# Kernel optimization log

Hardware: AMD Instinct MI355X
Metric: run time of the kernel (lower is better)

Reference implementation:

```python
import jax, jax.numpy as jnp
import numpy as np

N_HEAD, D_MODEL, D_HEAD = 16, 1024, 64
SEQ, BATCH = 2048, 2
EPS = 1e-5


def layer_norm(x, g, b):
    mu = jnp.mean(x, axis=-1, keepdims=True)
    var = jnp.var(x, axis=-1, keepdims=True)
    return (x - mu) * jax.lax.rsqrt(var + EPS) * g + b


def pos_table(n_rows, d_model):
    pos = jnp.arange(n_rows, dtype=jnp.float32)[:, None]
    freqs = jnp.power(10000.0, -jnp.arange(0, d_model, 2, dtype=jnp.float32) / d_model)
    ang = pos * freqs  # [n_rows, d_model//2]
    tab = jnp.zeros((n_rows, d_model), dtype=jnp.float32)
    tab = tab.at[:, 0::2].set(jnp.sin(ang))
    tab = tab.at[:, 1::2].set(jnp.cos(ang))
    return tab


def setup_inputs() -> dict:
    key = jax.random.key(0)
    ks = jax.random.split(key, 7)
    s = 0.02
    return {
        "dec_inp": jax.random.normal(ks[0], (SEQ, BATCH, D_MODEL), jnp.float32),
        "Wq": jax.random.normal(ks[1], (N_HEAD * D_HEAD, D_MODEL), jnp.float32) * s,
        "Wkv": jax.random.normal(ks[2], (2 * N_HEAD * D_HEAD, D_MODEL), jnp.float32) * s,
        "Wo": jax.random.normal(ks[3], (D_MODEL, N_HEAD * D_HEAD), jnp.float32) * s,
        "g1": jnp.ones((D_MODEL,), jnp.float32),
        "b1": jnp.zeros((D_MODEL,), jnp.float32),
        "Wff": jax.random.normal(ks[4], (D_MODEL, N_HEAD * D_HEAD), jnp.float32) * s,
        "g2": jnp.ones((D_MODEL,), jnp.float32),
        "b2": jnp.zeros((D_MODEL,), jnp.float32),
    }


def reference(dec_inp, Wq, Wkv, Wo, g1, b1, Wff, g2, b2):
    S, B, D = dec_inp.shape
    scale = 1.0 / (D_HEAD ** 0.5)
    # projections (post-lnorm path, no mems: c == h)
    q = jnp.einsum('ibd,ed->ibe', dec_inp, Wq).reshape(S, B, N_HEAD, D_HEAD)
    kv = jnp.einsum('ibd,ed->ibe', dec_inp, Wkv)
    k, v = jnp.split(kv, 2, axis=-1)
    k = k.reshape(S, B, N_HEAD, D_HEAD)
    v = v.reshape(S, B, N_HEAD, D_HEAD)
    # attention: scores [i, j, b, n], softmax over j (dim=1)
    scores = jnp.einsum('ibnd,jbnd->ijbn', q, k) * scale
    prob = jax.nn.softmax(scores, axis=1)
    vec = jnp.einsum('ijbn,jbnd->ibnd', prob, v).reshape(S, B, N_HEAD * D_HEAD)
    attn_out = jnp.einsum('ibe,de->ibd', vec, Wo)
    out = layer_norm(dec_inp + attn_out, g1, b1)
    # output += ff(output)
    out = out + jnp.einsum('ibe,de->ibd', out, Wff)
    out = layer_norm(out, g2, b2)
    # output += pos_emb(output)  ==  2*out + pe  (pe indexed by shape[1]==batch)
    pe = pos_table(B, D)  # [B, D], broadcasts over seq
    return out + (out + pe)
```

## Files before the change

### kernel.cpp

```cpp
#include <hip/hip_runtime.h>
#include <hip/hip_bf16.h>
#include <math.h>


typedef __bf16 bf16x8 __attribute__((ext_vector_type(8)));
typedef float f32x4  __attribute__((ext_vector_type(4)));

typedef const __attribute__((address_space(1))) unsigned int as1_uint;
typedef __attribute__((address_space(3))) unsigned int as3_uint;

constexpr int S_SEQ = 2048;
constexpr int DH    = 64;

#define WS_MB (1ull << 20)

__device__ __forceinline__ void gload16(void* lds, const void* g) {
  __builtin_amdgcn_global_load_lds((as1_uint*)g, (as3_uint*)lds, 16, 0, 0);
}

__device__ __forceinline__ float fast_exp2(float x) {
  float r;
  asm volatile("v_exp_f32 %0, %1\n\ts_nop 1" : "=v"(r) : "v"(x));
  return r;
}
__device__ __forceinline__ unsigned cvt_pk_bf16(float lo, float hi) {
  unsigned r;
  asm("v_cvt_pk_bf16_f32 %0, %1, %2" : "=v"(r) : "v"(lo), "v"(hi));
  return r;
}

__device__ __forceinline__ void cvt4(const float* __restrict__ in,
                                     __hip_bfloat16* __restrict__ out, int idx) {
  float4 v = ((const float4*)in)[idx];
  uint2 p;
  p.x = cvt_pk_bf16(v.x, v.y);
  p.y = cvt_pk_bf16(v.z, v.w);
  *(uint2*)(out + (size_t)idx * 4) = p;
}

__global__ __launch_bounds__(256)
void prep_kernel(const float* __restrict__ x, const float* __restrict__ Wq,
                 const float* __restrict__ Wkv, const float* __restrict__ Wo,
                 const float* __restrict__ Wff,
                 __hip_bfloat16* __restrict__ Xb,
                 __hip_bfloat16* __restrict__ Wqkv_b,
                 __hip_bfloat16* __restrict__ Wo_b,
                 __hip_bfloat16* __restrict__ Wff_b,
                 float* __restrict__ pe) {
  const int bid = blockIdx.x, t = threadIdx.x;
  if (bid < 4096) {
    cvt4(x, Xb, bid * 256 + t);
  } else if (bid < 5120) {
    cvt4(Wq, Wqkv_b, (bid - 4096) * 256 + t);
  } else if (bid < 7168) {
    cvt4(Wkv, Wqkv_b + 1024 * 1024, (bid - 5120) * 256 + t);
  } else if (bid < 8192) {
    cvt4(Wo, Wo_b, (bid - 7168) * 256 + t);
  } else if (bid < 9216) {
    cvt4(Wff, Wff_b, (bid - 8192) * 256 + t);
  } else {
#pragma unroll
    for (int rep = 0; rep < 2; ++rep) {
      const int k = rep * 256 + t;
      float freq = expf(-(2.0f * (float)k / 1024.0f) * logf(10000.0f));
      pe[2 * k]            = 0.0f;
      pe[2 * k + 1]        = 1.0f;
      pe[1024 + 2 * k]     = sinf(freq);
      pe[1024 + 2 * k + 1] = cosf(freq);
    }
  }
}

template <int MODE, int BN>
__global__ __launch_bounds__(256)
void gemm_bt(const __hip_bfloat16* __restrict__ A,
             const __hip_bfloat16* __restrict__ Bw,
             float* __restrict__ C,
             __hip_bfloat16* __restrict__ Qb,
             __hip_bfloat16* __restrict__ Kb,
             __hip_bfloat16* __restrict__ VTb,
             int Ndim, int Kdim) {
  constexpr int ASZ = 128 * 64 * 2;
  constexpr int BSZ = BN * 64 * 2;
  constexpr int NI  = BN / 32;
  __shared__ __align__(16) char smem[2 * (ASZ + BSZ)];
  const int t = threadIdx.x, w = t >> 6, l = t & 63;
  const int bm = blockIdx.y * 128, bn = blockIdx.x * BN;
  const int m0 = (w >> 1) * 64, n0 = (w & 1) * (BN / 2);
  const int lrow = l >> 3, lcol = l & 7;
  const int ll = l & 15, lg = l >> 4;

  auto stage = [&](char* buf, int kt) {
#pragma unroll
    for (int r = 0; r < 4; ++r) {
      const int chunk = r * 4 + w;
      const int row = chunk * 8 + lrow;
      gload16(buf + chunk * 1024 + l * 16,
              A + (size_t)(bm + row) * Kdim + kt + lcol * 8);
    }
#pragma unroll
    for (int r = 0; r < BN / 32; ++r) {
      const int chunk = r * 4 + w;
      const int row = chunk * 8 + lrow;
      gload16(buf + ASZ + chunk * 1024 + l * 16,
              Bw + (size_t)(bn + row) * Kdim + kt + lcol * 8);
    }
  };

  f32x4 acc[4][NI] = {};

  stage(smem, 0);
  __syncthreads();
  int cur = 0;
  for (int kt = 0; kt < Kdim; kt += 64) {
    char* bufc = smem + cur * (ASZ + BSZ);
    if (kt + 64 < Kdim) stage(smem + (cur ^ 1) * (ASZ + BSZ), kt + 64);
    const char* sA = bufc;
    const char* sB = bufc + ASZ;
#pragma unroll
    for (int ks = 0; ks < 2; ++ks) {
      bf16x8 a[4], bfr[NI];
#pragma unroll
      for (int mi = 0; mi < 4; ++mi)
        a[mi] = *(const bf16x8*)(sA + (m0 + mi * 16 + ll) * 128 + ks * 64 + lg * 16);
#pragma unroll
      for (int ni = 0; ni < NI; ++ni)
        bfr[ni] = *(const bf16x8*)(sB + (n0 + ni * 16 + ll) * 128 + ks * 64 + lg * 16);
#pragma unroll
      for (int mi = 0; mi < 4; ++mi)
#pragma unroll
        for (int ni = 0; ni < NI; ++ni)
          acc[mi][ni] = __builtin_amdgcn_mfma_f32_16x16x32_bf16(
              a[mi], bfr[ni], acc[mi][ni], 0, 0, 0);
    }
    __syncthreads();
    cur ^= 1;
  }

  if (MODE == 0) {
#pragma unroll
    for (int mi = 0; mi < 4; ++mi)
#pragma unroll
      for (int ni = 0; ni < NI; ++ni)
#pragma unroll
        for (int r = 0; r < 4; ++r) {
          const int gm = bm + m0 + mi * 16 + lg * 4 + r;
          const int gn = bn + n0 + ni * 16 + ll;
          C[(size_t)gm * Ndim + gn] = acc[mi][ni][r];
        }
  } else {
    __hip_bfloat16* img = (__hip_bfloat16*)smem;
    const bool isV = (bn >= 2048);
#pragma unroll
    for (int mi = 0; mi < 4; ++mi)
#pragma unroll
      for (int ni = 0; ni < NI; ++ni)
#pragma unroll
        for (int r = 0; r < 4; ++r) {
          const int gml = m0 + mi * 16 + lg * 4 + r;
          const int gnl = n0 + ni * 16 + ll;
          const int off = isV ? gnl * 136 + ((gml & 1) << 6) + (gml >> 1)
                              : gml * 136 + gnl;
          img[off] = __float2bfloat16(acc[mi][ni][r]);
        }
    __syncthreads();
    const int i0 = bm >> 1;
    const int tile0 = bm >> 6;
#pragma unroll
    for (int j = 0; j < 8; ++j) {
      const int c = j * 256 + t;
      uint4 val;
      __hip_bfloat16* dst;
      if (bn < 1024) {
        const int bb = c >> 10, hl = (c >> 9) & 1;
        const int q = c & 511, il = q >> 3, dh0 = (q & 7) * 8;
        val = *(const uint4*)&img[(il * 2 + bb) * 136 + hl * 64 + dh0];
        dst = Qb + ((size_t)(bb * 16 + (bn >> 6) + hl) * 2048 + i0 + il) * 64 + dh0;
      } else if (bn < 2048) {
        const int run = c >> 6, lane = c & 63;
        const int bb = run >> 4, hl = (run >> 3) & 1, th = (run >> 2) & 1,
                  instr = run & 3;
        const int lg2 = lane >> 4, ll2 = lane & 15;
        const int r32 = (ll2 >> 2) * 8 + (ll2 & 3) + ((instr >> 1) << 2);
        const int il = th * 32 + r32;
        const int dh0 = (instr & 1) * 32 + lg2 * 8;
        val = *(const uint4*)&img[(il * 2 + bb) * 136 + hl * 64 + dh0];
        dst = Kb + (size_t)(bb * 16 + ((bn - 1024) >> 6) + hl) * 131072 +
              (size_t)(tile0 + th) * 2048 + instr * 512 + lane * 8;
      } else {
        const int run = c >> 6, lane = c & 63;
        const int bb = run >> 4, hl = (run >> 3) & 1, th = (run >> 2) & 1,
                  df = run & 3;
        const int lg2 = lane >> 4, ll2 = lane & 15;
        const int il0 = th * 32 + lg2 * 8;
        const int gnl = hl * 64 + df * 16 + ll2;
        val = *(const uint4*)&img[gnl * 136 + bb * 64 + il0];
        dst = VTb + (size_t)(bb * 16 + ((bn - 2048) >> 6) + hl) * 131072 +
              (size_t)(tile0 + th) * 2048 + df * 512 + lane * 8;
      }
      *(uint4*)dst = val;
    }
  }
}


#define MFMA_B16 __builtin_amdgcn_mfma_f32_16x16x32_bf16

#define STAGE2(bufp, cb)                                                      \
  {                                                                           \
    gload16((bufp) + woff, Kf + (cb) + wl16);                                 \
    gload16((bufp) + 4096 + woff, Vf + (cb) + wl16);                          \
    gload16((bufp) + 8192 + woff, Kf + (cb) + 4096 + wl16);                   \
    gload16((bufp) + 12288 + woff, Vf + (cb) + 4096 + wl16);                  \
  }

#define COMPUTE(cur)                                                          \
  {                                                                           \
    bf16x8 kk[4], vv[4];                                                      \
    _Pragma("unroll")                                                         \
    for (int i = 0; i < 4; ++i) {                                             \
      kk[i] = *(const bf16x8*)((cur) + i * 1024 + l16);                       \
      vv[i] = *(const bf16x8*)((cur) + 4096 + i * 1024 + l16);                \
    }                                                                         \
    const f32x4 z = {0.f, 0.f, 0.f, 0.f};                                     \
    f32x4 s0[2], s1[2];                                                       \
    __builtin_amdgcn_s_setprio(1);                                            \
    s0[0] = MFMA_B16(kk[0], qf[0][0], z, 0, 0, 0);                            \
    s0[0] = MFMA_B16(kk[1], qf[0][1], s0[0], 0, 0, 0);                        \
    s1[0] = MFMA_B16(kk[2], qf[0][0], z, 0, 0, 0);                            \
    s1[0] = MFMA_B16(kk[3], qf[0][1], s1[0], 0, 0, 0);                        \
    s0[1] = MFMA_B16(kk[0], qf[1][0], z, 0, 0, 0);                            \
    s0[1] = MFMA_B16(kk[1], qf[1][1], s0[1], 0, 0, 0);                        \
    s1[1] = MFMA_B16(kk[2], qf[1][0], z, 0, 0, 0);                            \
    s1[1] = MFMA_B16(kk[3], qf[1][1], s1[1], 0, 0, 0);                        \
    __builtin_amdgcn_s_setprio(0);                                            \
    _Pragma("unroll")                                                         \
    for (int qi = 0; qi < 2; ++qi) {                                          \
      float p[8];                                                             \
      _Pragma("unroll")                                                       \
      for (int r = 0; r < 4; ++r) {                                           \
        p[r]     = fast_exp2(s0[qi][r] * C1);                                 \
        p[4 + r] = fast_exp2(s1[qi][r] * C1);                                 \
      }                                                                       \
      union { unsigned u[4]; bf16x8 v; } pk;                                  \
      pk.u[0] = cvt_pk_bf16(p[0], p[1]);                                      \
      pk.u[1] = cvt_pk_bf16(p[2], p[3]);                                      \
      pk.u[2] = cvt_pk_bf16(p[4], p[5]);                                      \
      pk.u[3] = cvt_pk_bf16(p[6], p[7]);                                      \
      __builtin_amdgcn_s_setprio(1);                                          \
      _Pragma("unroll")                                                       \
      for (int df = 0; df < 4; ++df)                                          \
        oacc[qi][df] = MFMA_B16(pk.v, vv[df], oacc[qi][df], 0, 0, 0);         \
      oaccS[qi] = MFMA_B16(pk.v, onesv.v, oaccS[qi], 0, 0, 0);                \
      __builtin_amdgcn_s_setprio(0);                                          \
    }                                                                         \
  }

#define PHASE(curbuf, stgbuf, stgoff, vmN_, doStage_)                         \
  {                                                                           \
    asm volatile("s_waitcnt vmcnt(" #vmN_ ")" ::: "memory");                  \
    __builtin_amdgcn_s_barrier();                                             \
    if (doStage_) STAGE2(stgbuf, stgoff);                                     \
    COMPUTE(curbuf);                                                          \
    COMPUTE((curbuf) + 8192);                                                 \
  }

__global__ __launch_bounds__(256)
void attn_kernel(const __hip_bfloat16* __restrict__ Qb,
                 const __hip_bfloat16* __restrict__ Kb,
                 const __hip_bfloat16* __restrict__ VTb,
                 __hip_bfloat16* __restrict__ vec) {
  __shared__ __align__(16) char lds[3 * 16384];
  const int t = threadIdx.x, w = t >> 6, l = t & 63;
  const int bid = blockIdx.x;
  const int slot = bid >> 3;
  const int bh = (bid & 7) * 4 + (slot & 3);
  const int qt = slot >> 2;
  const int b = bh >> 4, h = bh & 15;
  const __hip_bfloat16* Q = Qb + (size_t)bh * S_SEQ * DH;
  const char* Kf = (const char*)Kb + (size_t)bh * 262144;
  const char* Vf = (const char*)VTb + (size_t)bh * 262144;
  const int ll = l & 15, lg = l >> 4;
  const int l16 = l * 16;
  const int woff = w * 1024 + l16;
  const int wl16 = woff;
  constexpr float C1 = 0.125f * 1.44269504088896f;

  const int qbase = qt * 128 + w * 32;
  bf16x8 qf[2][2];
#pragma unroll
  for (int qi = 0; qi < 2; ++qi) {
    qf[qi][0] = *(const bf16x8*)(Q + (size_t)(qbase + qi * 16 + ll) * 64 + lg * 8);
    qf[qi][1] = *(const bf16x8*)(Q + (size_t)(qbase + qi * 16 + ll) * 64 + 32 + lg * 8);
  }

  union { unsigned u[4]; bf16x8 v; } onesv;
  onesv.u[0] = 0x3F803F80u; onesv.u[1] = 0x3F803F80u;
  onesv.u[2] = 0x3F803F80u; onesv.u[3] = 0x3F803F80u;

  f32x4 oacc[2][4] = {};
  f32x4 oaccS[2] = {};

  char* b0 = lds;
  char* b1 = lds + 16384;
  char* b2 = lds + 32768;

  STAGE2(b0, 0);
  STAGE2(b1, 8192);

  int cb = 2 * 8192;
  for (int i = 0; i < 10; ++i) {
    PHASE(b0, b2, cb, 4, true); cb += 8192;
    PHASE(b1, b0, cb, 4, true); cb += 8192;
    PHASE(b2, b1, cb, 4, true); cb += 8192;
  }
  PHASE(b0, b2, 0, 4, false);
  PHASE(b1, b0, 0, 0, false);

#pragma unroll
  for (int qi = 0; qi < 2; ++qi) {
    float invR[4];
#pragma unroll
    for (int r = 0; r < 4; ++r) invR[r] = 1.0f / oaccS[qi][r];
#pragma unroll
    for (int df = 0; df < 4; ++df)
#pragma unroll
      for (int r = 0; r < 4; ++r) {
        const int row = qbase + qi * 16 + 4 * lg + r;
        const int e = h * 64 + df * 16 + ll;
        vec[((size_t)row * 2 + b) * 1024 + e] =
            __float2bfloat16(oacc[qi][df][r] * invR[r]);
      }
  }
}

__global__ __launch_bounds__(256)
void add_ln_kernel(const float* __restrict__ X, const float* __restrict__ Yadd,
                   const float* __restrict__ g, const float* __restrict__ bb,
                   float* __restrict__ out_f32,
                   __hip_bfloat16* __restrict__ out_b16) {
  const int row = blockIdx.x, t = threadIdx.x;
  const float4 x4 = *(const float4*)(X + (size_t)row * 1024 + t * 4);
  const float4 a4 = *(const float4*)(Yadd + (size_t)row * 1024 + t * 4);
  float v[4] = {x4.x + a4.x, x4.y + a4.y, x4.z + a4.z, x4.w + a4.w};
  float s = v[0] + v[1] + v[2] + v[3];
  float s2 = v[0] * v[0] + v[1] * v[1] + v[2] * v[2] + v[3] * v[3];
#pragma unroll
  for (int off = 1; off < 64; off <<= 1) {
    s += __shfl_xor(s, off);
    s2 += __shfl_xor(s2, off);
  }
  __shared__ float rs[4], rs2[4];
  if ((t & 63) == 0) { rs[t >> 6] = s; rs2[t >> 6] = s2; }
  __syncthreads();
  const float tot = rs[0] + rs[1] + rs[2] + rs[3];
  const float tot2 = rs2[0] + rs2[1] + rs2[2] + rs2[3];
  const float mu = tot * (1.0f / 1024.0f);
  const float var = tot2 * (1.0f / 1024.0f) - mu * mu;
  const float rstd = rsqrtf(var + 1e-5f);
  const float4 g4 = *(const float4*)(g + t * 4);
  const float4 b4 = *(const float4*)(bb + t * 4);
  float y[4];
  y[0] = (v[0] - mu) * rstd * g4.x + b4.x;
  y[1] = (v[1] - mu) * rstd * g4.y + b4.y;
  y[2] = (v[2] - mu) * rstd * g4.z + b4.z;
  y[3] = (v[3] - mu) * rstd * g4.w + b4.w;
  *(float4*)(out_f32 + (size_t)row * 1024 + t * 4) =
      make_float4(y[0], y[1], y[2], y[3]);
  uint2 pk2;
  pk2.x = cvt_pk_bf16(y[0], y[1]);
  pk2.y = cvt_pk_bf16(y[2], y[3]);
  *(uint2*)(out_b16 + (size_t)row * 1024 + t * 4) = pk2;
}

__global__ __launch_bounds__(256)
void final_kernel(const float* __restrict__ X, const float* __restrict__ Yadd,
                  const float* __restrict__ g, const float* __restrict__ bb,
                  const float* __restrict__ pe, float* __restrict__ out) {
  const int row = blockIdx.x, t = threadIdx.x;
  const float4 x4 = *(const float4*)(X + (size_t)row * 1024 + t * 4);
  const float4 a4 = *(const float4*)(Yadd + (size_t)row * 1024 + t * 4);
  float v[4] = {x4.x + a4.x, x4.y + a4.y, x4.z + a4.z, x4.w + a4.w};
  float s = v[0] + v[1] + v[2] + v[3];
  float s2 = v[0] * v[0] + v[1] * v[1] + v[2] * v[2] + v[3] * v[3];
#pragma unroll
  for (int off = 1; off < 64; off <<= 1) {
    s += __shfl_xor(s, off);
    s2 += __shfl_xor(s2, off);
  }
  __shared__ float rs[4], rs2[4];
  if ((t & 63) == 0) { rs[t >> 6] = s; rs2[t >> 6] = s2; }
  __syncthreads();
  const float tot = rs[0] + rs[1] + rs[2] + rs[3];
  const float tot2 = rs2[0] + rs2[1] + rs2[2] + rs2[3];
  const float mu = tot * (1.0f / 1024.0f);
  const float var = tot2 * (1.0f / 1024.0f) - mu * mu;
  const float rstd = rsqrtf(var + 1e-5f);
  const float4 g4 = *(const float4*)(g + t * 4);
  const float4 b4 = *(const float4*)(bb + t * 4);
  const int bidx = row & 1;
  const float4 p4 = *(const float4*)(pe + bidx * 1024 + t * 4);
  float y[4];
  y[0] = 2.0f * ((v[0] - mu) * rstd * g4.x + b4.x) + p4.x;
  y[1] = 2.0f * ((v[1] - mu) * rstd * g4.y + b4.y) + p4.y;
  y[2] = 2.0f * ((v[2] - mu) * rstd * g4.z + b4.z) + p4.z;
  y[3] = 2.0f * ((v[3] - mu) * rstd * g4.w + b4.w) + p4.w;
  *(float4*)(out + (size_t)row * 1024 + t * 4) = make_float4(y[0], y[1], y[2], y[3]);
}

extern "C" void kernel_launch(void* const* d_in, const int* in_sizes, int n_in,
                              void* d_out, int out_size, void* d_ws,
                              size_t ws_size, hipStream_t stream) {
  const float* x   = (const float*)d_in[0];
  const float* Wq  = (const float*)d_in[1];
  const float* Wkv = (const float*)d_in[2];
  const float* Wo  = (const float*)d_in[3];
  const float* g1  = (const float*)d_in[4];
  const float* b1  = (const float*)d_in[5];
  const float* Wff = (const float*)d_in[6];
  const float* g2  = (const float*)d_in[7];
  const float* b2  = (const float*)d_in[8];

  char* ws = (char*)d_ws;
  __hip_bfloat16* Wqkv_b = (__hip_bfloat16*)(ws + 0);
  __hip_bfloat16* Wo_b   = (__hip_bfloat16*)(ws + 6 * WS_MB);
  __hip_bfloat16* Wff_b  = (__hip_bfloat16*)(ws + 8 * WS_MB);
  __hip_bfloat16* Xb     = (__hip_bfloat16*)(ws + 10 * WS_MB);
  __hip_bfloat16* Qb     = (__hip_bfloat16*)(ws + 18 * WS_MB);
  __hip_bfloat16* Kb     = (__hip_bfloat16*)(ws + 26 * WS_MB);
  __hip_bfloat16* VTb    = (__hip_bfloat16*)(ws + 34 * WS_MB);
  __hip_bfloat16* vecb   = (__hip_bfloat16*)(ws + 42 * WS_MB);
  float* attn            = (float*)(ws + 18 * WS_MB);
  float* out1            = (float*)(ws + 50 * WS_MB);
  __hip_bfloat16* out1b  = (__hip_bfloat16*)(ws + 66 * WS_MB);
  float* ffb             = (float*)(ws + 34 * WS_MB);
  float* pe              = (float*)(ws + 74 * WS_MB);

  prep_kernel<<<9217, 256, 0, stream>>>(x, Wq, Wkv, Wo, Wff, Xb, Wqkv_b,
                                        Wo_b, Wff_b, pe);
  gemm_bt<1, 128><<<dim3(24, 32), 256, 0, stream>>>(Xb, Wqkv_b, nullptr, Qb,
                                                    Kb, VTb, 3072, 1024);
  attn_kernel<<<dim3(512), 256, 0, stream>>>(Qb, Kb, VTb, vecb);
  gemm_bt<0, 64><<<dim3(16, 32), 256, 0, stream>>>(vecb, Wo_b, attn, nullptr,
                                                   nullptr, nullptr, 1024, 1024);
  add_ln_kernel<<<4096, 256, 0, stream>>>(x, attn, g1, b1, out1, out1b);
  gemm_bt<0, 64><<<dim3(16, 32), 256, 0, stream>>>(out1b, Wff_b, ffb, nullptr,
                                                   nullptr, nullptr, 1024, 1024);
  final_kernel<<<4096, 256, 0, stream>>>(out1, ffb, g2, b2, pe, (float*)d_out);
}
```

Baseline: 153.5 us.

## XOR-swizzle GEMM LDS tiles and prefetch two stages ahead with vmcnt waits

The bf16 GEMM kernel now applies an XOR swizzle to the 16-byte chunk column when loading global data into LDS, and reads fragments back with the matching swizzle. The aim is to cut LDS bank conflicts on the MFMA fragment reads. The K-loop is also restructured to issue loads two tiles ahead and wait on partial vmcnt counts with raw s_barrier instead of full __syncthreads, so global-to-LDS transfers overlap more with compute. The hand-tuned vmcnt constants depend on the load count per stage and on the compiler not reordering, which is a correctness risk if either changes.

```diff
diff --git a/kernel.cpp b/kernel.cpp
--- a/kernel.cpp
+++ b/kernel.cpp
@@ -89,6 +89,7 @@
   const int m0 = (w >> 1) * 64, n0 = (w & 1) * (BN / 2);
   const int lrow = l >> 3, lcol = l & 7;
   const int ll = l & 15, lg = l >> 4;
+  const int scol = (lcol ^ lrow) * 8;
 
   auto stage = [&](char* buf, int kt) {
 #pragma unroll
@@ -96,36 +97,49 @@
       const int chunk = r * 4 + w;
       const int row = chunk * 8 + lrow;
       gload16(buf + chunk * 1024 + l * 16,
-              A + (size_t)(bm + row) * Kdim + kt + lcol * 8);
+              A + (size_t)(bm + row) * Kdim + kt + scol);
     }
 #pragma unroll
     for (int r = 0; r < BN / 32; ++r) {
       const int chunk = r * 4 + w;
       const int row = chunk * 8 + lrow;
       gload16(buf + ASZ + chunk * 1024 + l * 16,
-              Bw + (size_t)(bn + row) * Kdim + kt + lcol * 8);
+              Bw + (size_t)(bn + row) * Kdim + kt + scol);
     }
   };
 
   f32x4 acc[4][NI] = {};
 
   stage(smem, 0);
-  __syncthreads();
-  int cur = 0;
-  for (int kt = 0; kt < Kdim; kt += 64) {
-    char* bufc = smem + cur * (ASZ + BSZ);
-    if (kt + 64 < Kdim) stage(smem + (cur ^ 1) * (ASZ + BSZ), kt + 64);
-    const char* sA = bufc;
-    const char* sB = bufc + ASZ;
+  stage(smem + (ASZ + BSZ), 64);
+  const int NST = Kdim / 64;
+  for (int kt = 0; kt < NST; ++kt) {
+    if (kt < NST - 1) {
+      if constexpr (BN == 128)
+        asm volatile("s_waitcnt vmcnt(8)" ::: "memory");
+      else
+        asm volatile("s_waitcnt vmcnt(6)" ::: "memory");
+    } else {
+      asm volatile("s_waitcnt vmcnt(0)" ::: "memory");
+    }
+    __builtin_amdgcn_s_barrier();
+    char* sA = smem + (kt & 1) * (ASZ + BSZ);
+    const char* sB = sA + ASZ;
 #pragma unroll
     for (int ks = 0; ks < 2; ++ks) {
       bf16x8 a[4], bfr[NI];
 #pragma unroll
-      for (int mi = 0; mi < 4; ++mi)
-        a[mi] = *(const bf16x8*)(sA + (m0 + mi * 16 + ll) * 128 + ks * 64 + lg * 16);
-#pragma unroll
-      for (int ni = 0; ni < NI; ++ni)
-        bfr[ni] = *(const bf16x8*)(sB + (n0 + ni * 16 + ll) * 128 + ks * 64 + lg * 16);
+      for (int mi = 0; mi < 4; ++mi) {
+        const int row = m0 + mi * 16 + ll;
+        a[mi] = *(const bf16x8*)(sA + row * 128 +
+                                 (((ks * 4 + lg) ^ (ll & 7)) << 4));
+      }
+#pragma unroll
+      for (int ni = 0; ni < NI; ++ni) {
+        const int row = n0 + ni * 16 + ll;
+        bfr[ni] = *(const bf16x8*)(sB + row * 128 +
+                                   (((ks * 4 + lg) ^ (ll & 7)) << 4));
+      }
 #pragma unroll
       for (int mi = 0; mi < 4; ++mi)
 #pragma unroll
@@ -133,8 +147,10 @@
           acc[mi][ni] = __builtin_amdgcn_mfma_f32_16x16x32_bf16(
               a[mi], bfr[ni], acc[mi][ni], 0, 0, 0);
     }
-    __syncthreads();
-    cur ^= 1;
+    if (kt + 2 < NST) {
+      __builtin_amdgcn_s_barrier();
+      stage(sA, (kt + 2) * 64);
+    }
   }
 
   if (MODE == 0) {
@@ -149,6 +165,7 @@
           C[(size_t)gm * Ndim + gn] = acc[mi][ni][r];
         }
   } else {
+    __syncthreads();
     __hip_bfloat16* img = (__hip_bfloat16*)smem;
     const bool isV = (bn >= 2048);
 #pragma unroll
```

After: 139.3 us. 1.1x faster.
